# Kernel optimization log

Hardware: AMD Instinct MI355X
Metric: run time of the kernel (lower is better)

The kernel has to match this reference:

```python
import jax, jax.numpy as jnp
import numpy as np

B, L, D = 32, 1024, 1024
H = 8            # hard-coded in FourierBlock weights1 leading dim
E = D // H       # 128
M = 64           # number of retained low-frequency modes
K = 25           # moving_avg kernel (stride 1)
PAD = (K - 1) // 2


def setup_inputs() -> dict:
    key = jax.random.key(0)
    ks = jax.random.split(key, 7)
    scale = 1.0 / (D * D)
    return {
        "x":   jax.random.normal(ks[0], (B, L, D), jnp.float32),
        "Wq":  jax.random.normal(ks[1], (D, D), jnp.float32) * 0.02,
        "bq":  jax.random.normal(ks[2], (D,), jnp.float32) * 0.02,
        "w1r": jax.random.uniform(ks[3], (H, E, E, M), jnp.float32) * scale,
        "w1i": jax.random.uniform(ks[4], (H, E, E, M), jnp.float32) * scale,
        "Wo":  jax.random.normal(ks[5], (D, D), jnp.float32) * 0.02,
        "bo":  jax.random.normal(ks[6], (D,), jnp.float32) * 0.02,
    }


def _forward(x, Wq, bq, w1r, w1i, Wo, bo):
    # --- AutoCorrelationLayer query projection (k,v projections are dead code in FourierBlock) ---
    q = (x @ Wq + bq).reshape(B, L, H, E)          # [B,L,H,E]
    # --- FourierBlock ---
    xq = q.transpose(0, 2, 3, 1)                   # [B,H,E,L]
    x_ft = jnp.fft.rfft(xq, axis=-1)               # [B,H,E,F], F=L//2+1, complex64
    w = w1r + 1j * w1i                             # [H,E,E,M]
    # mode_select='low': index = [0..M-1], output slot wi == i
    out_sel = jnp.einsum("bhem,heom->bhom", x_ft[..., :M], w)   # [B,H,E,M]
    F = L // 2 + 1
    out_ft = jnp.zeros((B, H, E, F), dtype=x_ft.dtype).at[..., :M].set(out_sel)
    y = jnp.fft.irfft(out_ft, n=L, axis=-1)        # [B,H,E,L] real
    # faithful to torch: .view(B, L, -1) on contiguous (B,H,E,L) = flat C-order reshape
    out = y.reshape(B, L, H * E)
    new_x = out @ Wo + bo                          # out_projection
    x2 = x + new_x                                 # dropout is identity in eval
    # --- series_decomp (moving average k=25, replicate padding, stride 1) ---
    xp = jnp.concatenate(
        [jnp.repeat(x2[:, :1], PAD, axis=1), x2, jnp.repeat(x2[:, -1:], PAD, axis=1)],
        axis=1)                                    # [B, L+2*PAD, D]
    cs = jnp.cumsum(xp, axis=1)
    cs = jnp.concatenate([jnp.zeros_like(cs[:, :1]), cs], axis=1)
    moving_mean = (cs[:, K:] - cs[:, :-K]) / K     # [B,L,D]
    res = x2 - moving_mean
    return res


def reference(x, Wq, bq, w1r, w1i, Wo, bo):
    # module returns (x, attn) with attn=None; we return the array output
    return _forward(x, Wq, bq, w1r, w1i, Wo, bo)
```

## Files before the change

kernel.cpp:

```cpp
#include <hip/hip_runtime.h>
#include <hip/hip_bf16.h>

typedef __bf16 bf16x8 __attribute__((ext_vector_type(8)));
typedef float f32x4 __attribute__((ext_vector_type(4)));
typedef unsigned short u16;
typedef unsigned int u32;
typedef unsigned long long u64;


static __device__ __forceinline__ u16 f2b(float f) {
  u32 u = __builtin_bit_cast(u32, f);
  u32 r = (u + 0x7FFFu + ((u >> 16) & 1u)) >> 16;
  return (u16)r;
}
static __device__ __forceinline__ float b2f(u16 s) {
  u32 u = ((u32)s) << 16;
  return __builtin_bit_cast(float, u);
}
static __device__ __forceinline__ f32x4 mfma16(bf16x8 a, bf16x8 b, f32x4 c) {
  return __builtin_amdgcn_mfma_f32_16x16x32_bf16(a, b, c, 0, 0, 0);
}

__global__ __launch_bounds__(256) void k_prep(
    const float* __restrict__ Wq, const float* __restrict__ Wo,
    u16* __restrict__ FT, u16* __restrict__ FI,
    u16* __restrict__ Wq16, u16* __restrict__ Wo16) {
  int idx = blockIdx.x * 256 + threadIdx.x;
  const float W0 = 6.283185307179586f / 1024.0f;
  if (idx < 131072) {
    int m2 = idx >> 10, l = idx & 1023;
    int m = (m2 < 64) ? m2 : (m2 - 64);
    int t = (m * l) & 1023;
    float s, c;
    __sincosf((float)t * W0, &s, &c);
    FT[idx] = f2b((m2 < 64) ? c : -s);
  } else if (idx < 262144) {
    int j = idx - 131072;
    int m2 = j >> 10, l = j & 1023;
    int m = (m2 < 64) ? m2 : (m2 - 64);
    int t = (m * l) & 1023;
    float s, c;
    __sincosf((float)t * W0, &s, &c);
    float v;
    if (m2 == 0) v = 1.0f / 1024.0f;
    else if (m2 < 64) v = c * (2.0f / 1024.0f);
    else if (m2 == 64) v = 0.0f;
    else v = -s * (2.0f / 1024.0f);
    FI[j] = f2b(v);
  } else if (idx < 262144 + 1048576) {
    int k = idx - 262144;
    Wq16[k] = f2b(Wq[k]);
  } else {
    int k = idx - 1310720;
    Wo16[k] = f2b(Wo[k]);
  }
}

__global__ __launch_bounds__(256) void k_wtrans(
    const float* __restrict__ w1r, const float* __restrict__ w1i,
    u16* __restrict__ W2r, u16* __restrict__ W2i) {
  __shared__ float T[128 * 65];
  int h = blockIdx.x >> 7, e = blockIdx.x & 127;
  int tid = threadIdx.x;
  for (int pass = 0; pass < 2; ++pass) {
    const float* src = pass ? w1i : w1r;
    u16* dst = pass ? W2i : W2r;
    {
      int m = tid & 63, og = tid >> 6;
      const float* sp = src + (((size_t)h * 128 + e) * 128) * 64 + m;
      for (int k = 0; k < 32; ++k) {
        int o = og * 32 + k;
        T[o * 65 + m] = sp[(size_t)o * 64];
      }
    }
    __syncthreads();
    {
      int o = tid & 127, mg = tid >> 7;
      for (int k = 0; k < 32; ++k) {
        int m = mg * 32 + k;
        dst[(((size_t)h * 64 + m) * 128 + e) * 128 + o] = f2b(T[o * 65 + m]);
      }
    }
    __syncthreads();
  }
}

template <int KSTEPS, bool BIAS>
static __device__ __forceinline__ void gemm128(
    const u16* __restrict__ A, size_t arow0, int astride,
    const u16* __restrict__ Bm, int bcol0,
    u16* __restrict__ C, size_t crow0, const float* __restrict__ bias) {
  __shared__ __align__(16) u16 Al[128 * 40];
  __shared__ __align__(16) u16 Bl[128 * 40];
  int tid = threadIdx.x, lane = tid & 63, w = tid >> 6;
  f32x4 acc[2][8];
#pragma unroll
  for (int i = 0; i < 2; i++)
#pragma unroll
    for (int j = 0; j < 8; j++) acc[i][j] = (f32x4){0.f, 0.f, 0.f, 0.f};
  int ar = tid >> 1, ahalf = tid & 1;
  int dloc = tid & 127, lg = tid >> 7;
  for (int kk = 0; kk < KSTEPS; ++kk) {
    {
      const uint4* src = (const uint4*)(A + (arow0 + ar) * (size_t)astride + kk * 32 + ahalf * 16);
      uint4 v0 = src[0], v1 = src[1];
      uint4* dst = (uint4*)(Al + ar * 40 + ahalf * 16);
      dst[0] = v0; dst[1] = v1;
    }
    {
#pragma unroll
      for (int jj = 0; jj < 4; ++jj) {
        int l0 = lg * 16 + jj * 4;
        const u16* bp = Bm + (size_t)(kk * 32 + l0) * 1024 + bcol0 + dloc;
        u16 s0 = bp[0], s1 = bp[1024], s2 = bp[2048], s3 = bp[3072];
        *(u64*)(Bl + dloc * 40 + l0) =
            (u64)s0 | ((u64)s1 << 16) | ((u64)s2 << 32) | ((u64)s3 << 48);
      }
    }
    __syncthreads();
    bf16x8 af[2];
#pragma unroll
    for (int mi = 0; mi < 2; mi++)
      af[mi] = *(const bf16x8*)(Al + (w * 32 + mi * 16 + (lane & 15)) * 40 + 8 * (lane >> 4));
#pragma unroll
    for (int ni = 0; ni < 8; ni++) {
      bf16x8 bf = *(const bf16x8*)(Bl + (ni * 16 + (lane & 15)) * 40 + 8 * (lane >> 4));
#pragma unroll
      for (int mi = 0; mi < 2; mi++) acc[mi][ni] = mfma16(af[mi], bf, acc[mi][ni]);
    }
    __syncthreads();
  }
  if (BIAS) {
    if (w == 0 && (lane >> 4) == 0) {
#pragma unroll
      for (int ni = 0; ni < 8; ni++)
        acc[0][ni][0] += 1024.0f * bias[bcol0 + ni * 16 + (lane & 15)];
    }
  }
#pragma unroll
  for (int mi = 0; mi < 2; mi++)
#pragma unroll
    for (int ni = 0; ni < 8; ni++)
#pragma unroll
      for (int r = 0; r < 4; r++) {
        int row = w * 32 + mi * 16 + 4 * (lane >> 4) + r;
        int col = bcol0 + ni * 16 + (lane & 15);
        C[(crow0 + row) * (size_t)1024 + col] = f2b(acc[mi][ni][r]);
      }
}

__global__ __launch_bounds__(256) void k_dft(const float* __restrict__ x,
                                             const u16* __restrict__ FT,
                                             u16* __restrict__ Z) {
  __shared__ __align__(16) u16 Al[128 * 40];
  __shared__ __align__(16) u16 Bl[128 * 40];
  int b = blockIdx.x >> 3, ct = blockIdx.x & 7;
  int tid = threadIdx.x, lane = tid & 63, w = tid >> 6;
  f32x4 acc[2][8];
#pragma unroll
  for (int i = 0; i < 2; i++)
#pragma unroll
    for (int j = 0; j < 8; j++) acc[i][j] = (f32x4){0.f, 0.f, 0.f, 0.f};
  int am2 = tid >> 1, ahalf = tid & 1;
  int c = tid & 127, lg = tid >> 7;
  for (int kk = 0; kk < 32; ++kk) {
    {
      const uint4* src = (const uint4*)(FT + am2 * 1024 + kk * 32 + ahalf * 16);
      uint4 v0 = src[0], v1 = src[1];
      uint4* dst = (uint4*)(Al + am2 * 40 + ahalf * 16);
      dst[0] = v0; dst[1] = v1;
    }
    {
      const float* xb = x + ((size_t)b * 1024 + kk * 32) * 1024 + ct * 128 + c;
#pragma unroll
      for (int jj = 0; jj < 4; ++jj) {
        int l0 = lg * 16 + jj * 4;
        float f0 = xb[(size_t)(l0 + 0) * 1024];
        float f1 = xb[(size_t)(l0 + 1) * 1024];
        float f2_ = xb[(size_t)(l0 + 2) * 1024];
        float f3 = xb[(size_t)(l0 + 3) * 1024];
        *(u64*)(Bl + c * 40 + l0) = (u64)f2b(f0) | ((u64)f2b(f1) << 16) |
                                    ((u64)f2b(f2_) << 32) | ((u64)f2b(f3) << 48);
      }
    }
    __syncthreads();
    bf16x8 af[2];
#pragma unroll
    for (int mi = 0; mi < 2; mi++)
      af[mi] = *(const bf16x8*)(Al + (w * 32 + mi * 16 + (lane & 15)) * 40 + 8 * (lane >> 4));
#pragma unroll
    for (int ni = 0; ni < 8; ni++) {
      bf16x8 bf = *(const bf16x8*)(Bl + (ni * 16 + (lane & 15)) * 40 + 8 * (lane >> 4));
#pragma unroll
      for (int mi = 0; mi < 2; mi++) acc[mi][ni] = mfma16(af[mi], bf, acc[mi][ni]);
    }
    __syncthreads();
  }
#pragma unroll
  for (int mi = 0; mi < 2; mi++)
#pragma unroll
    for (int ni = 0; ni < 8; ni++)
#pragma unroll
      for (int r = 0; r < 4; r++) {
        int row = w * 32 + mi * 16 + 4 * (lane >> 4) + r;
        int col = ct * 128 + ni * 16 + (lane & 15);
        Z[((size_t)b * 128 + row) * 1024 + col] = f2b(acc[mi][ni][r]);
      }
}

__global__ __launch_bounds__(256) void k_wqmix(const u16* __restrict__ Zm,
                                               const u16* __restrict__ Wq16,
                                               const float* __restrict__ bq,
                                               u16* __restrict__ XF) {
  int mt = blockIdx.x >> 3, nt = blockIdx.x & 7;
  gemm128<32, true>(Zm, (size_t)mt * 128, 1024, Wq16, nt * 128, XF, (size_t)mt * 128, bq);
}

__global__ __launch_bounds__(256) void k_gmat(const u16* __restrict__ FI,
                                              const u16* __restrict__ Wo16,
                                              u16* __restrict__ G) {
  int nt = blockIdx.x;
  gemm128<32, false>(FI, 0, 1024, Wo16, nt * 128, G, 0, nullptr);
}

__global__ __launch_bounds__(256) void k_modemix(const u16* __restrict__ XF,
                                                 const u16* __restrict__ W2r,
                                                 const u16* __restrict__ W2i,
                                                 u16* __restrict__ OS2T) {
  __shared__ __align__(16) u16 XAr[32 * 200], XAi[32 * 200];
  __shared__ __align__(16) u16 Wbr[128 * 40], Wbi[128 * 40];
  int h = blockIdx.x >> 6, m = blockIdx.x & 63;
  int tid = threadIdx.x, lane = tid & 63, w = tid >> 6;
  {
    int bb = tid >> 3, seg = tid & 7;
    int e0 = seg * 16, kc = seg >> 1, off = (seg & 1) * 16;
    const uint4* sr = (const uint4*)(XF + ((size_t)bb * 128 + m) * 1024 + h * 128 + e0);
    const uint4* si = (const uint4*)(XF + ((size_t)bb * 128 + 64 + m) * 1024 + h * 128 + e0);
    uint4* dr = (uint4*)(XAr + bb * 200 + kc * 40 + off);
    uint4* di = (uint4*)(XAi + bb * 200 + kc * 40 + off);
    dr[0] = sr[0]; dr[1] = sr[1];
    di[0] = si[0]; di[1] = si[1];
  }
  f32x4 accR[2][2], accI[2][2];
#pragma unroll
  for (int i = 0; i < 2; i++)
#pragma unroll
    for (int j = 0; j < 2; j++) {
      accR[i][j] = (f32x4){0.f, 0.f, 0.f, 0.f};
      accI[i][j] = (f32x4){0.f, 0.f, 0.f, 0.f};
    }
  for (int kk = 0; kk < 4; ++kk) {
    {
      int o = tid & 127, pr = tid >> 7;
      const u16* src = (pr ? W2i : W2r) + (((size_t)h * 64 + m) * 128 + kk * 32) * 128 + o;
      u16* dst = (pr ? Wbi : Wbr) + o * 40;
#pragma unroll
      for (int jj = 0; jj < 8; ++jj) {
        int e0 = jj * 4;
        u16 s0 = src[(size_t)(e0 + 0) * 128], s1 = src[(size_t)(e0 + 1) * 128];
        u16 s2 = src[(size_t)(e0 + 2) * 128], s3 = src[(size_t)(e0 + 3) * 128];
        *(u64*)(dst + e0) = (u64)s0 | ((u64)s1 << 16) | ((u64)s2 << 32) | ((u64)s3 << 48);
      }
    }
    __syncthreads();
    bf16x8 ar[2], ai_[2], ain[2];
#pragma unroll
    for (int mi = 0; mi < 2; mi++) {
      int bb = mi * 16 + (lane & 15);
      ar[mi] = *(const bf16x8*)(XAr + bb * 200 + kk * 40 + 8 * (lane >> 4));
      ai_[mi] = *(const bf16x8*)(XAi + bb * 200 + kk * 40 + 8 * (lane >> 4));
      u32 t4[4];
      __builtin_memcpy(t4, &ai_[mi], 16);
#pragma unroll
      for (int q = 0; q < 4; q++) t4[q] ^= 0x80008000u;
      __builtin_memcpy(&ain[mi], t4, 16);
    }
#pragma unroll
    for (int ni = 0; ni < 2; ni++) {
      int o = w * 32 + ni * 16 + (lane & 15);
      bf16x8 br = *(const bf16x8*)(Wbr + o * 40 + 8 * (lane >> 4));
      bf16x8 bi = *(const bf16x8*)(Wbi + o * 40 + 8 * (lane >> 4));
#pragma unroll
      for (int mi = 0; mi < 2; mi++) {
        accR[mi][ni] = mfma16(ar[mi], br, accR[mi][ni]);
        accR[mi][ni] = mfma16(ain[mi], bi, accR[mi][ni]);
        accI[mi][ni] = mfma16(ar[mi], bi, accI[mi][ni]);
        accI[mi][ni] = mfma16(ai_[mi], br, accI[mi][ni]);
      }
    }
    __syncthreads();
  }
#pragma unroll
  for (int mi = 0; mi < 2; mi++)
#pragma unroll
    for (int ni = 0; ni < 2; ni++)
#pragma unroll
      for (int rr = 0; rr < 4; rr++) {
        int brow = mi * 16 + 4 * (lane >> 4) + rr;
        int o = w * 32 + ni * 16 + (lane & 15);
        size_t base = (size_t)brow * 131072 + (size_t)(h * 128 + o) * 128;
        OS2T[base + m] = f2b(accR[mi][ni][rr]);
        OS2T[base + 64 + m] = f2b(accI[mi][ni][rr]);
      }
}

__global__ __launch_bounds__(256) void k_osg(const u16* __restrict__ OS2T,
                                             const u16* __restrict__ G,
                                             u16* __restrict__ NX) {
  int b = blockIdx.x >> 6, t6 = blockIdx.x & 63;
  int mt = t6 >> 3, nt = t6 & 7;
  gemm128<4, false>(OS2T, (size_t)b * 1024 + mt * 128, 128, G, nt * 128, NX,
                    (size_t)b * 1024 + mt * 128, nullptr);
}

__global__ __launch_bounds__(256) void k_decomp(const float* __restrict__ x,
                                                const u16* __restrict__ NX,
                                                float* __restrict__ out) {
  __shared__ float ZT[280 * 64];
  int b = blockIdx.x >> 6, r6 = blockIdx.x & 63;
  int lc = r6 >> 4, dt = r6 & 15;
  int tid = threadIdx.x, dl = tid & 63;
  int l0 = lc * 256, dbase = dt * 64;
  for (int r = tid >> 6; r < 280; r += 4) {
    int gl = l0 + r - 12;
    gl = gl < 0 ? 0 : (gl > 1023 ? 1023 : gl);
    size_t gi = ((size_t)b * 1024 + gl) * 1024 + dbase + dl;
    ZT[r * 64 + dl] = x[gi] + b2f(NX[gi]);
  }
  __syncthreads();
  int sub = tid >> 6;
  int base = sub * 64;
  float s = 0.0f;
#pragma unroll
  for (int j = 0; j < 25; ++j) s += ZT[(base + j) * 64 + dl];
  for (int i = 0; i < 64; ++i) {
    float center = ZT[(base + i + 12) * 64 + dl];
    size_t oi = ((size_t)b * 1024 + l0 + base + i) * 1024 + dbase + dl;
    out[oi] = center - s * (1.0f / 25.0f);
    if (i < 63) s += ZT[(base + i + 25) * 64 + dl] - ZT[(base + i) * 64 + dl];
  }
}

extern "C" void kernel_launch(void* const* d_in, const int* in_sizes, int n_in,
                              void* d_out, int out_size, void* d_ws, size_t ws_size,
                              hipStream_t stream) {
  const float* x = (const float*)d_in[0];
  const float* Wq = (const float*)d_in[1];
  const float* bq = (const float*)d_in[2];
  const float* w1r = (const float*)d_in[3];
  const float* w1i = (const float*)d_in[4];
  const float* Wo = (const float*)d_in[5];

  char* ws = (char*)d_ws;
  u16* FT = (u16*)(ws + 0x000000);
  u16* FI = (u16*)(ws + 0x040000);
  u16* Wq16 = (u16*)(ws + 0x080000);
  u16* Wo16 = (u16*)(ws + 0x280000);
  u16* G = (u16*)(ws + 0x480000);
  u16* NX = (u16*)(ws + 0x500000);

  char* ob = (char*)d_out;
  u16* W2r = (u16*)(ob + 0x0000000);
  u16* W2i = (u16*)(ob + 0x1000000);
  u16* Zm = (u16*)(ob + 0x2000000);
  u16* XF = (u16*)(ob + 0x2800000);
  u16* OS2T = (u16*)(ob + 0x3000000);

  k_prep<<<9216, 256, 0, stream>>>(Wq, Wo, FT, FI, Wq16, Wo16);
  k_wtrans<<<1024, 256, 0, stream>>>(w1r, w1i, W2r, W2i);
  k_gmat<<<8, 256, 0, stream>>>(FI, Wo16, G);
  k_dft<<<256, 256, 0, stream>>>(x, FT, Zm);
  k_wqmix<<<256, 256, 0, stream>>>(Zm, Wq16, bq, XF);
  k_modemix<<<512, 256, 0, stream>>>(XF, W2r, W2i, OS2T);
  k_osg<<<2048, 256, 0, stream>>>(OS2T, G, NX);
  k_decomp<<<2048, 256, 0, stream>>>(x, NX, (float*)d_out);
}
```

Baseline: 487.7 us.

## Fuse inverse-DFT output GEMM with residual add and moving-average decomposition

Merges the OS2T×G GEMM (k_osg) and the series-decomposition kernel into one kernel, k_nxdecomp. Each block computes a 160-row halo tile of new_x with MFMA, adds x in registers, stages the sum in shared memory and applies the 25-tap sliding window directly, so the bf16 NX intermediate never goes to HBM. To allow contiguous loads, the inverse-DFT matrix rows and the mode-mix output are interleaved as real/imag pairs, and OS2T moves into the workspace. The cost is about 25% redundant GEMM work for the halo rows, plus duplicated x reads across row tiles.

```diff
diff --git a/kernel.cpp b/kernel.cpp
--- a/kernel.cpp
+++ b/kernel.cpp
@@ -17,13 +17,16 @@
   u32 u = ((u32)s) << 16;
   return __builtin_bit_cast(float, u);
 }
+static __device__ __forceinline__ u32 pk2(float lo, float hi) {
+  return (u32)f2b(lo) | ((u32)f2b(hi) << 16);
+}
 static __device__ __forceinline__ f32x4 mfma16(bf16x8 a, bf16x8 b, f32x4 c) {
   return __builtin_amdgcn_mfma_f32_16x16x32_bf16(a, b, c, 0, 0, 0);
 }
 
 __global__ __launch_bounds__(256) void k_prep(
     const float* __restrict__ Wq, const float* __restrict__ Wo,
-    u16* __restrict__ FT, u16* __restrict__ FI,
+    u16* __restrict__ FT, u16* __restrict__ FI2,
     u16* __restrict__ Wq16, u16* __restrict__ Wo16) {
   int idx = blockIdx.x * 256 + threadIdx.x;
   const float W0 = 6.283185307179586f / 1024.0f;
@@ -35,18 +38,16 @@
     __sincosf((float)t * W0, &s, &c);
     FT[idx] = f2b((m2 < 64) ? c : -s);
   } else if (idx < 262144) {
-    int j = idx - 131072;
-    int m2 = j >> 10, l = j & 1023;
-    int m = (m2 < 64) ? m2 : (m2 - 64);
+    int jj = idx - 131072;
+    int j = jj >> 10, l = jj & 1023;
+    int m = j >> 1;
     int t = (m * l) & 1023;
     float s, c;
     __sincosf((float)t * W0, &s, &c);
     float v;
-    if (m2 == 0) v = 1.0f / 1024.0f;
-    else if (m2 < 64) v = c * (2.0f / 1024.0f);
-    else if (m2 == 64) v = 0.0f;
-    else v = -s * (2.0f / 1024.0f);
-    FI[j] = f2b(v);
+    if ((j & 1) == 0) v = (m == 0) ? (1.0f / 1024.0f) : c * (2.0f / 1024.0f);
+    else              v = (m == 0) ? 0.0f : -s * (2.0f / 1024.0f);
+    FI2[jj] = f2b(v);
   } else if (idx < 262144 + 1048576) {
     int k = idx - 262144;
     Wq16[k] = f2b(Wq[k]);
@@ -179,8 +180,8 @@
         float f1 = xb[(size_t)(l0 + 1) * 1024];
         float f2_ = xb[(size_t)(l0 + 2) * 1024];
         float f3 = xb[(size_t)(l0 + 3) * 1024];
-        *(u64*)(Bl + c * 40 + l0) = (u64)f2b(f0) | ((u64)f2b(f1) << 16) |
-                                    ((u64)f2b(f2_) << 32) | ((u64)f2b(f3) << 48);
+        uint2 p = {pk2(f0, f1), pk2(f2_, f3)};
+        *(uint2*)(Bl + c * 40 + l0) = p;
       }
     }
     __syncthreads();
@@ -216,11 +217,11 @@
   gemm128<32, true>(Zm, (size_t)mt * 128, 1024, Wq16, nt * 128, XF, (size_t)mt * 128, bq);
 }
 
-__global__ __launch_bounds__(256) void k_gmat(const u16* __restrict__ FI,
+__global__ __launch_bounds__(256) void k_gmat(const u16* __restrict__ FI2,
                                               const u16* __restrict__ Wo16,
-                                              u16* __restrict__ G) {
+                                              u16* __restrict__ G2) {
   int nt = blockIdx.x;
-  gemm128<32, false>(FI, 0, 1024, Wo16, nt * 128, G, 0, nullptr);
+  gemm128<32, false>(FI2, 0, 1024, Wo16, nt * 128, G2, 0, nullptr);
 }
 
 __global__ __launch_bounds__(256) void k_modemix(const u16* __restrict__ XF,
@@ -299,45 +300,101 @@
         int brow = mi * 16 + 4 * (lane >> 4) + rr;
         int o = w * 32 + ni * 16 + (lane & 15);
         size_t base = (size_t)brow * 131072 + (size_t)(h * 128 + o) * 128;
-        OS2T[base + m] = f2b(accR[mi][ni][rr]);
-        OS2T[base + 64 + m] = f2b(accI[mi][ni][rr]);
-      }
-}
-
-__global__ __launch_bounds__(256) void k_osg(const u16* __restrict__ OS2T,
-                                             const u16* __restrict__ G,
-                                             u16* __restrict__ NX) {
-  int b = blockIdx.x >> 6, t6 = blockIdx.x & 63;
-  int mt = t6 >> 3, nt = t6 & 7;
-  gemm128<4, false>(OS2T, (size_t)b * 1024 + mt * 128, 128, G, nt * 128, NX,
-                    (size_t)b * 1024 + mt * 128, nullptr);
-}
-
-__global__ __launch_bounds__(256) void k_decomp(const float* __restrict__ x,
-                                                const u16* __restrict__ NX,
-                                                float* __restrict__ out) {
-  __shared__ float ZT[280 * 64];
-  int b = blockIdx.x >> 6, r6 = blockIdx.x & 63;
-  int lc = r6 >> 4, dt = r6 & 15;
-  int tid = threadIdx.x, dl = tid & 63;
-  int l0 = lc * 256, dbase = dt * 64;
-  for (int r = tid >> 6; r < 280; r += 4) {
-    int gl = l0 + r - 12;
-    gl = gl < 0 ? 0 : (gl > 1023 ? 1023 : gl);
-    size_t gi = ((size_t)b * 1024 + gl) * 1024 + dbase + dl;
-    ZT[r * 64 + dl] = x[gi] + b2f(NX[gi]);
-  }
+        *(u32*)(OS2T + base + 2 * m) = pk2(accR[mi][ni][rr], accI[mi][ni][rr]);
+      }
+}
+
+__global__ __launch_bounds__(256) void k_nxdecomp(const float* __restrict__ x,
+                                                  const u16* __restrict__ OS2T,
+                                                  const u16* __restrict__ G2,
+                                                  float* __restrict__ out) {
+  __shared__ __align__(16) u16 SMEM[160 * 136 + 64 * 136];
+  u16* Al = SMEM;
+  u16* Bl = SMEM + 160 * 136;
+  float* ZT = (float*)SMEM;
+  int bid = blockIdx.x;
+  int rt = bid & 7, dt = (bid >> 3) & 15, b = bid >> 7;
+  int r0 = rt * 128, d0 = dt * 64;
+  int tid = threadIdx.x, lane = tid & 63, w = tid >> 6;
+  int wr = w >> 1, wc = w & 1;
+  for (int it = 0; it < 10; ++it) {
+    int q = tid + it * 256;
+    int row = q >> 4, seg = q & 15;
+    int gr = r0 - 16 + row;
+    gr = gr < 0 ? 0 : (gr > 1023 ? 1023 : gr);
+    *(uint4*)(Al + row * 136 + seg * 8) =
+        *(const uint4*)(OS2T + ((size_t)b * 1024 + gr) * 128 + seg * 8);
+  }
+  {
+    int c = tid & 63, lg = tid >> 6;
+#pragma unroll
+    for (int jj = 0; jj < 8; ++jj) {
+      int l0 = lg * 32 + jj * 4;
+      const u16* gp = G2 + (size_t)l0 * 1024 + d0 + c;
+      u16 s0 = gp[0], s1 = gp[1024], s2 = gp[2048], s3 = gp[3072];
+      *(u64*)(Bl + c * 136 + l0) =
+          (u64)s0 | ((u64)s1 << 16) | ((u64)s2 << 32) | ((u64)s3 << 48);
+    }
+  }
+  float xv[5][2][4];
+#pragma unroll
+  for (int mi = 0; mi < 5; ++mi)
+#pragma unroll
+    for (int r = 0; r < 4; ++r) {
+      int row = wr * 80 + mi * 16 + 4 * (lane >> 4) + r;
+      int gr = r0 - 16 + row;
+      gr = gr < 0 ? 0 : (gr > 1023 ? 1023 : gr);
+#pragma unroll
+      for (int ni = 0; ni < 2; ++ni) {
+        int col = wc * 32 + ni * 16 + (lane & 15);
+        xv[mi][ni][r] = x[((size_t)b * 1024 + gr) * 1024 + d0 + col];
+      }
+    }
+  f32x4 acc[5][2];
+#pragma unroll
+  for (int i = 0; i < 5; i++)
+#pragma unroll
+    for (int j = 0; j < 2; j++) acc[i][j] = (f32x4){0.f, 0.f, 0.f, 0.f};
   __syncthreads();
-  int sub = tid >> 6;
-  int base = sub * 64;
-  float s = 0.0f;
-#pragma unroll
-  for (int j = 0; j < 25; ++j) s += ZT[(base + j) * 64 + dl];
-  for (int i = 0; i < 64; ++i) {
-    float center = ZT[(base + i + 12) * 64 + dl];
-    size_t oi = ((size_t)b * 1024 + l0 + base + i) * 1024 + dbase + dl;
-    out[oi] = center - s * (1.0f / 25.0f);
-    if (i < 63) s += ZT[(base + i + 25) * 64 + dl] - ZT[(base + i) * 64 + dl];
+#pragma unroll
+  for (int kk = 0; kk < 4; ++kk) {
+    bf16x8 af[5], bf[2];
+#pragma unroll
+    for (int mi = 0; mi < 5; ++mi)
+      af[mi] = *(const bf16x8*)(Al + (wr * 80 + mi * 16 + (lane & 15)) * 136 +
+                                kk * 32 + 8 * (lane >> 4));
+#pragma unroll
+    for (int ni = 0; ni < 2; ++ni)
+      bf[ni] = *(const bf16x8*)(Bl + (wc * 32 + ni * 16 + (lane & 15)) * 136 +
+                                kk * 32 + 8 * (lane >> 4));
+#pragma unroll
+    for (int mi = 0; mi < 5; ++mi)
+#pragma unroll
+      for (int ni = 0; ni < 2; ++ni) acc[mi][ni] = mfma16(af[mi], bf[ni], acc[mi][ni]);
+  }
+  __syncthreads();
+#pragma unroll
+  for (int mi = 0; mi < 5; ++mi)
+#pragma unroll
+    for (int ni = 0; ni < 2; ++ni)
+#pragma unroll
+      for (int r = 0; r < 4; ++r) {
+        int row = wr * 80 + mi * 16 + 4 * (lane >> 4) + r;
+        int col = wc * 32 + ni * 16 + (lane & 15);
+        ZT[row * 68 + col] = acc[mi][ni][r] + xv[mi][ni][r];
+      }
+  __syncthreads();
+  {
+    int c = tid & 63, h2 = tid >> 6;
+    int j0 = h2 * 32;
+    float s = 0.f;
+#pragma unroll
+    for (int u = 0; u < 25; ++u) s += ZT[(j0 + 4 + u) * 68 + c];
+    for (int j = j0; j < j0 + 32; ++j) {
+      float center = ZT[(j + 16) * 68 + c];
+      out[((size_t)b * 1024 + r0 + j) * 1024 + d0 + c] = center - s * (1.0f / 25.0f);
+      if (j < j0 + 31) s += ZT[(j + 29) * 68 + c] - ZT[(j + 4) * 68 + c];
+    }
   }
 }
 
@@ -353,25 +410,23 @@
 
   char* ws = (char*)d_ws;
   u16* FT = (u16*)(ws + 0x000000);
-  u16* FI = (u16*)(ws + 0x040000);
+  u16* FI2 = (u16*)(ws + 0x040000);
   u16* Wq16 = (u16*)(ws + 0x080000);
   u16* Wo16 = (u16*)(ws + 0x280000);
-  u16* G = (u16*)(ws + 0x480000);
-  u16* NX = (u16*)(ws + 0x500000);
+  u16* G2 = (u16*)(ws + 0x480000);
+  u16* OS2T = (u16*)(ws + 0x4C0000);
 
   char* ob = (char*)d_out;
   u16* W2r = (u16*)(ob + 0x0000000);
   u16* W2i = (u16*)(ob + 0x1000000);
   u16* Zm = (u16*)(ob + 0x2000000);
   u16* XF = (u16*)(ob + 0x2800000);
-  u16* OS2T = (u16*)(ob + 0x3000000);
-
-  k_prep<<<9216, 256, 0, stream>>>(Wq, Wo, FT, FI, Wq16, Wo16);
+
+  k_prep<<<9216, 256, 0, stream>>>(Wq, Wo, FT, FI2, Wq16, Wo16);
   k_wtrans<<<1024, 256, 0, stream>>>(w1r, w1i, W2r, W2i);
-  k_gmat<<<8, 256, 0, stream>>>(FI, Wo16, G);
+  k_gmat<<<8, 256, 0, stream>>>(FI2, Wo16, G2);
   k_dft<<<256, 256, 0, stream>>>(x, FT, Zm);
   k_wqmix<<<256, 256, 0, stream>>>(Zm, Wq16, bq, XF);
   k_modemix<<<512, 256, 0, stream>>>(XF, W2r, W2i, OS2T);
-  k_osg<<<2048, 256, 0, stream>>>(OS2T, G, NX);
-  k_decomp<<<2048, 256, 0, stream>>>(x, NX, (float*)d_out);
-}
+  k_nxdecomp<<<4096, 256, 0, stream>>>(x, OS2T, G2, (float*)d_out);
+}
```

New measurement: 429.4 us. -12.0%, faster.
